# Performance work log

Hardware: AMD Instinct MI355X
Metric: run time of the kernel (lower is better)

Reference implementation:

```python
import jax, jax.numpy as jnp
import numpy as np

B = 4; D = H = W = 28; C = 192; NH = 6; WS = 7; SS = 3
L = D * H * W; N = WS ** 3; HD = C // NH


def _rel_index():
    c = np.stack(np.meshgrid(np.arange(WS), np.arange(WS), np.arange(WS), indexing='ij')).reshape(3, -1)
    r = c[:, :, None] - c[:, None, :] + (WS - 1)
    return jnp.asarray(r[0] * (2 * WS - 1) ** 2 + r[1] * (2 * WS - 1) + r[2])  # (N,N)


def _attn_mask():
    img = np.zeros((D, H, W), np.float32)
    sl = (slice(0, -WS), slice(-WS, -SS), slice(-SS, None))
    cnt = 0
    for d in sl:
        for h in sl:
            for w in sl:
                img[d, h, w] = cnt; cnt += 1
    mw = img.reshape(D // WS, WS, H // WS, WS, W // WS, WS).transpose(0, 2, 4, 1, 3, 5).reshape(-1, N)
    am = mw[:, None, :] - mw[:, :, None]
    return jnp.asarray(np.where(am != 0, -100.0, 0.0).astype(np.float32))  # (nW,N,N)

REL_IDX = _rel_index()
ATTN_MASK = _attn_mask()


def _ln(x, g, b):
    m = x.mean(-1, keepdims=True)
    v = ((x - m) ** 2).mean(-1, keepdims=True)
    return (x - m) / jnp.sqrt(v + 1e-5) * g + b


def _window_partition(x):  # (B,D,H,W,C) -> (B*nW, N, C)
    x = x.reshape(B, D // WS, WS, H // WS, WS, W // WS, WS, C)
    return x.transpose(0, 1, 3, 5, 2, 4, 6, 7).reshape(-1, N, C)


def _window_reverse(w):  # (B*nW, N, C) -> (B,D,H,W,C)
    x = w.reshape(B, D // WS, H // WS, W // WS, WS, WS, WS, C)
    return x.transpose(0, 1, 4, 2, 5, 3, 6, 7).reshape(B, D, H, W, C)


def setup_inputs() -> dict:
    key = jax.random.key(0)
    ks = jax.random.split(key, 8)
    s = 0.02
    return {
        'x': jax.random.normal(ks[0], (B, L, C), jnp.float32),
        'norm1_g': jnp.ones((C,), jnp.float32), 'norm1_b': jnp.zeros((C,), jnp.float32),
        'qkv_w': jax.random.normal(ks[1], (3 * C, C), jnp.float32) * s,
        'qkv_b': jnp.zeros((3 * C,), jnp.float32),
        'proj_w': jax.random.normal(ks[2], (C, C), jnp.float32) * s,
        'proj_b': jnp.zeros((C,), jnp.float32),
        'rel_table': jax.random.normal(ks[3], ((2 * WS - 1) ** 3, NH), jnp.float32) * s,
        'norm2_g': jnp.ones((C,), jnp.float32), 'norm2_b': jnp.zeros((C,), jnp.float32),
        'fc1_w': jax.random.normal(ks[4], (4 * C, C), jnp.float32) * s,
        'fc1_b': jnp.zeros((4 * C,), jnp.float32),
        'fc2_w': jax.random.normal(ks[5], (C, 4 * C), jnp.float32) * s,
        'fc2_b': jnp.zeros((C,), jnp.float32),
    }


def reference(x, norm1_g, norm1_b, qkv_w, qkv_b, proj_w, proj_b, rel_table,
              norm2_g, norm2_b, fc1_w, fc1_b, fc2_w, fc2_b):
    shortcut = x
    h = _ln(x, norm1_g, norm1_b).reshape(B, D, H, W, C)
    h = jnp.roll(h, (-SS, -SS, -SS), axis=(1, 2, 3))
    xw = _window_partition(h)                                  # (B_, N, C)
    B_ = xw.shape[0]
    qkv = (xw @ qkv_w.T + qkv_b).reshape(B_, N, 3, NH, HD).transpose(2, 0, 3, 1, 4)
    q, k, v = qkv[0], qkv[1], qkv[2]                           # (B_, NH, N, HD)
    attn = jnp.einsum('bhnd,bhmd->bhnm', q * (HD ** -0.5), k)
    bias = rel_table[REL_IDX].transpose(2, 0, 1)               # (NH, N, N)
    attn = attn + bias[None]
    nW = ATTN_MASK.shape[0]
    attn = (attn.reshape(B, nW, NH, N, N) + ATTN_MASK[None, :, None]).reshape(B_, NH, N, N)
    attn = jax.nn.softmax(attn, axis=-1)
    out = jnp.einsum('bhnm,bhmd->bhnd', attn, v).transpose(0, 2, 1, 3).reshape(B_, N, C)
    out = out @ proj_w.T + proj_b
    h = _window_reverse(out)
    h = jnp.roll(h, (SS, SS, SS), axis=(1, 2, 3)).reshape(B, L, C)
    x = shortcut + h
    y = _ln(x, norm2_g, norm2_b)
    y = jax.nn.gelu(y @ fc1_w.T + fc1_b, approximate=False)
    return x + (y @ fc2_w.T + fc2_b)
```

## Files before the change

kernel.cpp:

```cpp
#include <hip/hip_runtime.h>

#define DEV __device__ __forceinline__

typedef __bf16 bf16x8 __attribute__((ext_vector_type(8)));
typedef float f32x4 __attribute__((ext_vector_type(4)));

DEV float bflo(unsigned int u) { union { unsigned int x; float f; } c; c.x = u << 16; return c.f; }
DEV unsigned short f2bf(float f) {
  union { float f; unsigned int u; } c; c.f = f;
  unsigned int u = c.u;
  return (unsigned short)((u + 0x7fffu + ((u >> 16) & 1u)) >> 16);
}
DEV unsigned int pkbf(float a, float b) {
  unsigned int r;
  asm("v_cvt_pk_bf16_f32 %0, %1, %2" : "=v"(r) : "v"(a), "v"(b));
  return r;
}
DEV float gelu_fast(float y) {
  float y2 = y * y;
  float z = y * fmaf(y2, 0.10294348f, 2.30220842f);
  float e = __builtin_amdgcn_exp2f(z);
  float r = __builtin_amdgcn_rcpf(e + 1.0f);
  return fmaf(-y, r, y);
}

DEV void gload16(const void* g, void* l) {
  __builtin_amdgcn_global_load_lds((const __attribute__((address_space(1))) void*)g,
                                   (__attribute__((address_space(3))) void*)l, 16, 0, 0);
}

__global__ __launch_bounds__(256) void wconv_all(const float* __restrict__ s0,
                                                 const float* __restrict__ s1,
                                                 const float* __restrict__ s2,
                                                 const float* __restrict__ s3,
                                                 unsigned short* __restrict__ dst) {
  int i = blockIdx.x * 256 + threadIdx.x;
  const float* src; int off, real;
  if (i < 122880)      { src = s0; off = i;          real = 110592; }
  else if (i < 172032) { src = s1; off = i - 122880; real = 36864; }
  else if (i < 319488) { src = s2; off = i - 172032; real = 147456; }
  else                 { src = s3; off = i - 319488; real = 147456; }
  dst[i] = (off < real) ? f2bf(src[off]) : (unsigned short)0;
}

__global__ __launch_bounds__(256) void bmt_kernel(const float* __restrict__ rel_table,
                                                  unsigned short* __restrict__ bmt4) {
  int wth = blockIdx.x;
  int wt = wth / 6, h = wth - wt * 6;
  int r = blockIdx.y;
  unsigned short* row = bmt4 + (((size_t)wth * 88 + r) * 352) * 4;
  for (int q = threadIdx.x; q < 352; q += 256) {
    int mb_q = 0, cls_q = 0;
    bool qv = q < 343;
    if (qv) {
      int ii_q = q / 49, rem_q = q - ii_q * 49;
      int jj_q = rem_q / 7, ww_q = rem_q - jj_q * 7;
      mb_q = ii_q * 169 + jj_q * 13 + ww_q;
      int cd_q = (wt & 4) ? (ii_q < 4 ? 1 : 2) : 0;
      int ch_q = (wt & 2) ? (jj_q < 4 ? 1 : 2) : 0;
      int cw_q = (wt & 1) ? (ww_q < 4 ? 1 : 2) : 0;
      cls_q = cd_q * 9 + ch_q * 3 + cw_q;
    }
    unsigned short ov[4];
#pragma unroll
    for (int i = 0; i < 4; i++) {
      int kk = 4 * r + i;
      float v;
      if (kk >= 343) v = -30000.f;
      else if (!qv) v = 0.f;
      else {
        int ii_k = kk / 49, rem_k = kk - ii_k * 49;
        int jj_k = rem_k / 7, ww_k = rem_k - jj_k * 7;
        int mb_k = ii_k * 169 + jj_k * 13 + ww_k;
        int cd_k = (wt & 4) ? (ii_k < 4 ? 1 : 2) : 0;
        int ch_k = (wt & 2) ? (jj_k < 4 ? 1 : 2) : 0;
        int cw_k = (wt & 1) ? (ww_k < 4 ? 1 : 2) : 0;
        int cls_k = cd_k * 9 + ch_k * 3 + cw_k;
        v = rel_table[(mb_q - mb_k + 1098) * 6 + h] * 1.4426950408889634f;
        if (cls_q != cls_k) v -= 144.26950408889634f;
      }
      ov[i] = f2bf(v);
    }
    unsigned int lo = (unsigned)ov[0] | ((unsigned)ov[1] << 16);
    unsigned int hi = (unsigned)ov[2] | ((unsigned)ov[3] << 16);
    *(uint2*)(row + q * 4) = make_uint2(lo, hi);
  }
}

__global__ __launch_bounds__(256) void ln_kernel(const float* __restrict__ x,
                                                 const float* __restrict__ g,
                                                 const float* __restrict__ b,
                                                 unsigned short* __restrict__ out) {
  int row = (blockIdx.x << 2) + (threadIdx.x >> 6);
  int lane = threadIdx.x & 63;
  int w_ = row / 343, n_ = row - w_ * 343;
  int bb = w_ >> 6, wrem = w_ & 63;
  int wd = wrem >> 4, wh = (wrem >> 2) & 3, ww = wrem & 3;
  int ii = n_ / 49, rem = n_ - ii * 49;
  int jj = rem / 7, kk = rem - jj * 7;
  int d = wd * 7 + ii + 3; if (d >= 28) d -= 28;
  int hh = wh * 7 + jj + 3; if (hh >= 28) hh -= 28;
  int wb = ww * 7 + kk + 3; if (wb >= 28) wb -= 28;
  const float* xr = x + ((size_t)bb * 21952 + (d * 28 + hh) * 28 + wb) * 192;
  float v0 = xr[lane], v1 = xr[lane + 64], v2 = xr[lane + 128];
  float s = v0 + v1 + v2;
  float sq = v0 * v0 + v1 * v1 + v2 * v2;
#pragma unroll
  for (int o = 32; o > 0; o >>= 1) {
    s += __shfl_xor(s, o, 64);
    sq += __shfl_xor(sq, o, 64);
  }
  float mean = s * (1.0f / 192.0f);
  float var = sq * (1.0f / 192.0f) - mean * mean;
  float rstd = rsqrtf(var + 1e-5f);
  unsigned short* orow = out + (size_t)row * 192;
  orow[lane]       = f2bf((v0 - mean) * rstd * g[lane] + b[lane]);
  orow[lane + 64]  = f2bf((v1 - mean) * rstd * g[lane + 64] + b[lane + 64]);
  orow[lane + 128] = f2bf((v2 - mean) * rstd * g[lane + 128] + b[lane + 128]);
}

__global__ __launch_bounds__(256) void gemm_qkv(
    const unsigned short* __restrict__ A, const unsigned short* __restrict__ W,
    const float* __restrict__ bias,
    unsigned short* __restrict__ oq, unsigned short* __restrict__ okk,
    unsigned short* __restrict__ ov) {
  __shared__ __align__(16) unsigned short As[2][128 * 64];
  __shared__ __align__(16) unsigned short Bs[2][128 * 64];
  const int K = 192;
  const int orig = blockIdx.x;
  const int xcd = orig & 7, off = orig >> 3;
  const int wgid = (xcd < 6 ? xcd * 429 : 2574 + (xcd - 6) * 428) + off;
  const int by = wgid / 5, bx = wgid - by * 5;
  const int bm = by << 7, bn = bx << 7;

  const int tid = threadIdx.x;
  const int lane = tid & 63;
  const int wv = tid >> 6;
  const int wr = wv >> 1, wc = wv & 1;
  const int l15 = lane & 15, l4 = lane >> 4;
  const int srow = lane >> 3;
  const int scole = ((lane & 7) ^ srow) << 3;

  f32x4 acc[4][4];
#pragma unroll
  for (int a = 0; a < 4; a++)
#pragma unroll
    for (int b2 = 0; b2 < 4; b2++) acc[a][b2] = (f32x4){0.f, 0.f, 0.f, 0.f};

  auto stage = [&](int kt, int buf) {
#pragma unroll
    for (int i = 0; i < 4; i++) {
      int c = (i << 2) + wv;
      int row = (c << 3) + srow;
      gload16(A + (size_t)(bm + row) * K + (kt << 6) + scole, &As[buf][c << 9]);
      gload16(W + (size_t)(bn + row) * K + (kt << 6) + scole, &Bs[buf][c << 9]);
    }
  };

  stage(0, 0);
  int cur = 0;
  for (int kt = 0; kt < 3; ++kt) {
    if (kt < 2) {
      stage(kt + 1, cur ^ 1);
      asm volatile("s_waitcnt vmcnt(8)" ::: "memory");
    } else {
      asm volatile("s_waitcnt vmcnt(0)" ::: "memory");
    }
    __builtin_amdgcn_s_barrier();
    __builtin_amdgcn_sched_barrier(0);
#pragma unroll
    for (int ks = 0; ks < 2; ks++) {
      bf16x8 af[4], bfr[4];
#pragma unroll
      for (int fm = 0; fm < 4; fm++) {
        int r = (wr << 6) + (fm << 4) + l15;
        int c = (ks << 2) + l4;
        af[fm] = *(const bf16x8*)(&As[cur][(r << 6) + ((c ^ (r & 7)) << 3)]);
      }
#pragma unroll
      for (int fn = 0; fn < 4; fn++) {
        int r = (wc << 6) + (fn << 4) + l15;
        int c = (ks << 2) + l4;
        bfr[fn] = *(const bf16x8*)(&Bs[cur][(r << 6) + ((c ^ (r & 7)) << 3)]);
      }
#pragma unroll
      for (int fm = 0; fm < 4; fm++)
#pragma unroll
        for (int fn = 0; fn < 4; fn++)
          acc[fm][fn] = __builtin_amdgcn_mfma_f32_16x16x32_bf16(bfr[fn], af[fm], acc[fm][fn], 0, 0, 0);
    }
    if (kt < 2) {
      __builtin_amdgcn_sched_barrier(0);
      __builtin_amdgcn_s_barrier();
      cur ^= 1;
    }
  }

#pragma unroll
  for (int fm = 0; fm < 4; fm++) {
    int gr = bm + (wr << 6) + (fm << 4) + l15;
    int w_ = gr / 343, n_ = gr - w_ * 343;
#pragma unroll
    for (int fn = 0; fn < 4; fn++) {
      int gc0 = bn + (wc << 6) + (fn << 4) + (l4 << 2);
      if (gc0 < 576) {
        float4 bv = *(const float4*)(bias + gc0);
        float v0 = acc[fm][fn][0] + bv.x, v1 = acc[fm][fn][1] + bv.y;
        float v2 = acc[fm][fn][2] + bv.z, v3 = acc[fm][fn][3] + bv.w;
        int which = gc0 / 192;
        int cc3 = gc0 - which * 192;
        int hh2 = cc3 >> 5, dd0 = cc3 & 31;
        size_t offo = ((size_t)(w_ * 6 + hh2) * 343 + n_) * 32 + dd0;
        if (which == 0) {
          const float sc = 0.17677669529663687f * 1.4426950408889634f;
          *(uint2*)(oq + offo) = make_uint2(pkbf(v0 * sc, v1 * sc), pkbf(v2 * sc, v3 * sc));
        } else if (which == 1) {
          *(uint2*)(okk + offo) = make_uint2(pkbf(v0, v1), pkbf(v2, v3));
        } else {
          *(uint2*)(ov + offo) = make_uint2(pkbf(v0, v1), pkbf(v2, v3));
        }
      }
    }
  }
}

__global__ __launch_bounds__(256) void gemm_proj_ln(
    const unsigned short* __restrict__ A, const unsigned short* __restrict__ W,
    const float* __restrict__ bias, const float* __restrict__ x,
    const float* __restrict__ g2, const float* __restrict__ b2,
    unsigned short* __restrict__ xnew, unsigned short* __restrict__ xw2) {
  __shared__ __align__(16) char smem[65536];
  unsigned short (*As)[64 * 64] = (unsigned short (*)[64 * 64])smem;
  unsigned short (*Bs)[192 * 64] = (unsigned short (*)[192 * 64])(smem + 16384);
  float* red = (float*)smem;

  const int tid = threadIdx.x;
  const int lane = tid & 63;
  const int wv = tid >> 6;
  const int bm = blockIdx.x << 6;
  const int l15 = lane & 15, l4 = lane >> 4;
  const int srow = lane >> 3;
  const int scole = ((lane & 7) ^ srow) << 3;
  const int K = 192;

  f32x4 acc[4][3];
#pragma unroll
  for (int a = 0; a < 4; a++)
#pragma unroll
    for (int b_ = 0; b_ < 3; b_++) acc[a][b_] = (f32x4){0.f, 0.f, 0.f, 0.f};

  auto stage = [&](int kt, int buf) {
#pragma unroll
    for (int i = 0; i < 2; i++) {
      int c = (i << 2) + wv;
      gload16(A + (size_t)(bm + (c << 3) + srow) * K + (kt << 6) + scole, &As[buf][c << 9]);
    }
#pragma unroll
    for (int i = 0; i < 6; i++) {
      int c = (i << 2) + wv;
      gload16(W + (size_t)((c << 3) + srow) * K + (kt << 6) + scole, &Bs[buf][c << 9]);
    }
  };

  stage(0, 0);
  int cur = 0;
  for (int kt = 0; kt < 3; ++kt) {
    if (kt < 2) {
      stage(kt + 1, cur ^ 1);
      asm volatile("s_waitcnt vmcnt(8)" ::: "memory");
    } else {
      asm volatile("s_waitcnt vmcnt(0)" ::: "memory");
    }
    __builtin_amdgcn_s_barrier();
    __builtin_amdgcn_sched_barrier(0);
#pragma unroll
    for (int ks = 0; ks < 2; ks++) {
      bf16x8 af[4], bfr[3];
#pragma unroll
      for (int fm = 0; fm < 4; fm++) {
        int r = (fm << 4) + l15;
        int c = (ks << 2) + l4;
        af[fm] = *(const bf16x8*)(&As[cur][(r << 6) + ((c ^ (r & 7)) << 3)]);
      }
#pragma unroll
      for (int fn = 0; fn < 3; fn++) {
        int r = (wv * 48) + (fn << 4) + l15;
        int c = (ks << 2) + l4;
        bfr[fn] = *(const bf16x8*)(&Bs[cur][(r << 6) + ((c ^ (r & 7)) << 3)]);
      }
#pragma unroll
      for (int fm = 0; fm < 4; fm++)
#pragma unroll
        for (int fn = 0; fn < 3; fn++)
          acc[fm][fn] = __builtin_amdgcn_mfma_f32_16x16x32_bf16(bfr[fn], af[fm], acc[fm][fn], 0, 0, 0);
    }
    if (kt < 2) {
      __builtin_amdgcn_sched_barrier(0);
      __builtin_amdgcn_s_barrier();
      cur ^= 1;
    }
  }

  size_t orow[4];
#pragma unroll
  for (int fm = 0; fm < 4; fm++) {
    int gr = bm + (fm << 4) + l15;
    int w_ = gr / 343, n_ = gr - w_ * 343;
    int bb = w_ >> 6, wrem = w_ & 63;
    int wd = wrem >> 4, wh = (wrem >> 2) & 3, ww = wrem & 3;
    int ii = n_ / 49, rem = n_ - ii * 49;
    int jj = rem / 7, kk = rem - jj * 7;
    int d = wd * 7 + ii + 3; if (d >= 28) d -= 28;
    int hh = wh * 7 + jj + 3; if (hh >= 28) hh -= 28;
    int wb = ww * 7 + kk + 3; if (wb >= 28) wb -= 28;
    orow[fm] = ((size_t)bb * 21952 + (d * 28 + hh) * 28 + wb) * 192;
  }
  float ps[4], psq[4];
#pragma unroll
  for (int fm = 0; fm < 4; fm++) {
    float s = 0.f, sq = 0.f;
#pragma unroll
    for (int fn = 0; fn < 3; fn++) {
      int gc0 = wv * 48 + (fn << 4) + (l4 << 2);
      float4 bv = *(const float4*)(bias + gc0);
      float4 xv = *(const float4*)(x + orow[fm] + gc0);
      acc[fm][fn][0] += bv.x + xv.x;
      acc[fm][fn][1] += bv.y + xv.y;
      acc[fm][fn][2] += bv.z + xv.z;
      acc[fm][fn][3] += bv.w + xv.w;
#pragma unroll
      for (int i = 0; i < 4; i++) {
        float v = acc[fm][fn][i];
        s += v; sq += v * v;
      }
    }
    ps[fm] = s; psq[fm] = sq;
  }
#pragma unroll
  for (int fm = 0; fm < 4; fm++) {
    ps[fm] += __shfl_xor(ps[fm], 16, 64);
    ps[fm] += __shfl_xor(ps[fm], 32, 64);
    psq[fm] += __shfl_xor(psq[fm], 16, 64);
    psq[fm] += __shfl_xor(psq[fm], 32, 64);
  }
  __syncthreads();
  if (l4 == 0) {
#pragma unroll
    for (int fm = 0; fm < 4; fm++) {
      int tr = (fm << 4) + l15;
      red[tr * 8 + wv] = ps[fm];
      red[tr * 8 + 4 + wv] = psq[fm];
    }
  }
  __syncthreads();
  if (tid < 64) {
    float s = red[tid * 8] + red[tid * 8 + 1] + red[tid * 8 + 2] + red[tid * 8 + 3];
    float sq = red[tid * 8 + 4] + red[tid * 8 + 5] + red[tid * 8 + 6] + red[tid * 8 + 7];
    float mean = s * (1.0f / 192.0f);
    float var = sq * (1.0f / 192.0f) - mean * mean;
    red[tid * 8] = mean;
    red[tid * 8 + 1] = rsqrtf(var + 1e-5f);
  }
  __syncthreads();
#pragma unroll
  for (int fm = 0; fm < 4; fm++) {
    int tr = (fm << 4) + l15;
    float mean = red[tr * 8], rstd = red[tr * 8 + 1];
#pragma unroll
    for (int fn = 0; fn < 3; fn++) {
      int gc0 = wv * 48 + (fn << 4) + (l4 << 2);
      float4 gv = *(const float4*)(g2 + gc0);
      float4 b2v = *(const float4*)(b2 + gc0);
      float v0 = acc[fm][fn][0], v1 = acc[fm][fn][1];
      float v2 = acc[fm][fn][2], v3 = acc[fm][fn][3];
      *(uint2*)(xnew + orow[fm] + gc0) = make_uint2(pkbf(v0, v1), pkbf(v2, v3));
      float y0 = (v0 - mean) * rstd * gv.x + b2v.x;
      float y1 = (v1 - mean) * rstd * gv.y + b2v.y;
      float y2 = (v2 - mean) * rstd * gv.z + b2v.z;
      float y3 = (v3 - mean) * rstd * gv.w + b2v.w;
      *(uint2*)(xw2 + orow[fm] + gc0) = make_uint2(pkbf(y0, y1), pkbf(y2, y3));
    }
  }
}

__global__ __launch_bounds__(256) void mlp_fused(
    const unsigned short* __restrict__ A,
    const unsigned short* __restrict__ W1,
    const float* __restrict__ b1,
    const unsigned short* __restrict__ W2,
    const float* __restrict__ b2,
    const unsigned short* __restrict__ residb,
    float* __restrict__ out) {
  __shared__ __align__(16) unsigned short As[64 * 192];
  __shared__ __align__(16) unsigned short Hs[64 * 264];
  const int tid = threadIdx.x, lane = tid & 63, wv = tid >> 6;
  const int l15 = lane & 15, l4 = lane >> 4;
  const int bm = blockIdx.x << 6;

#pragma unroll
  for (int i = 0; i < 6; i++) {
    int idx = i * 256 + tid;
    int r = idx / 24, c = idx - r * 24;
    gload16(A + (size_t)(bm + r) * 192 + ((c ^ (r & 7)) << 3), As + r * 192 + (c << 3));
  }

  f32x4 acc2[4][3];
#pragma unroll
  for (int a = 0; a < 4; a++)
#pragma unroll
    for (int b_ = 0; b_ < 3; b_++) acc2[a][b_] = (f32x4){0.f, 0.f, 0.f, 0.f};

  asm volatile("s_waitcnt vmcnt(0)" ::: "memory");
  __syncthreads();

  for (int cc = 0; cc < 3; cc++) {
    f32x4 acc1[4][4];
#pragma unroll
    for (int a = 0; a < 4; a++)
#pragma unroll
      for (int b_ = 0; b_ < 4; b_++) acc1[a][b_] = (f32x4){0.f, 0.f, 0.f, 0.f};
#pragma unroll
    for (int ks = 0; ks < 6; ks++) {
      bf16x8 af[4], bf[4];
#pragma unroll
      for (int fm = 0; fm < 4; fm++) {
        int r = (fm << 4) + l15;
        int ch = (ks << 2) + l4;
        af[fm] = *(const bf16x8*)(As + r * 192 + ((ch ^ (r & 7)) << 3));
      }
#pragma unroll
      for (int fn = 0; fn < 4; fn++) {
        int hrow = (cc << 8) + (wv << 6) + (fn << 4) + l15;
        bf[fn] = *(const bf16x8*)(W1 + (size_t)hrow * 192 + (ks << 5) + (l4 << 3));
      }
#pragma unroll
      for (int fm = 0; fm < 4; fm++)
#pragma unroll
        for (int fn = 0; fn < 4; fn++)
          acc1[fm][fn] = __builtin_amdgcn_mfma_f32_16x16x32_bf16(bf[fn], af[fm], acc1[fm][fn], 0, 0, 0);
    }
    __syncthreads();
#pragma unroll
    for (int fm = 0; fm < 4; fm++) {
      int r = (fm << 4) + l15;
#pragma unroll
      for (int fn = 0; fn < 4; fn++) {
        int hc = (wv << 6) + (fn << 4) + (l4 << 2);
        float4 bv = *(const float4*)(b1 + (cc << 8) + hc);
        float g0 = gelu_fast(acc1[fm][fn][0] + bv.x);
        float g1 = gelu_fast(acc1[fm][fn][1] + bv.y);
        float g2 = gelu_fast(acc1[fm][fn][2] + bv.z);
        float g3 = gelu_fast(acc1[fm][fn][3] + bv.w);
        *(uint2*)(Hs + r * 264 + hc) = make_uint2(pkbf(g0, g1), pkbf(g2, g3));
      }
    }
    __syncthreads();
#pragma unroll
    for (int ks = 0; ks < 8; ks++) {
      bf16x8 hf[4], wf[3];
#pragma unroll
      for (int fm = 0; fm < 4; fm++) {
        int r = (fm << 4) + l15;
        hf[fm] = *(const bf16x8*)(Hs + r * 264 + (ks << 5) + (l4 << 3));
      }
#pragma unroll
      for (int fn = 0; fn < 3; fn++) {
        int j = wv * 48 + (fn << 4) + l15;
        wf[fn] = *(const bf16x8*)(W2 + (size_t)j * 768 + (cc << 8) + (ks << 5) + (l4 << 3));
      }
#pragma unroll
      for (int fm = 0; fm < 4; fm++)
#pragma unroll
        for (int fn = 0; fn < 3; fn++)
          acc2[fm][fn] = __builtin_amdgcn_mfma_f32_16x16x32_bf16(wf[fn], hf[fm], acc2[fm][fn], 0, 0, 0);
    }
  }

#pragma unroll
  for (int fm = 0; fm < 4; fm++) {
    int gr = bm + (fm << 4) + l15;
#pragma unroll
    for (int fn = 0; fn < 3; fn++) {
      int gc0 = wv * 48 + (fn << 4) + (l4 << 2);
      size_t oi = (size_t)gr * 192 + gc0;
      float4 bv = *(const float4*)(b2 + gc0);
      uint2 rb = *(const uint2*)(residb + oi);
      float4 o;
      o.x = acc2[fm][fn][0] + bv.x + bflo(rb.x & 0xffffu);
      o.y = acc2[fm][fn][1] + bv.y + bflo(rb.x >> 16);
      o.z = acc2[fm][fn][2] + bv.z + bflo(rb.y & 0xffffu);
      o.w = acc2[fm][fn][3] + bv.w + bflo(rb.y >> 16);
      *(float4*)(out + oi) = o;
    }
  }
}

__global__ __launch_bounds__(256) void attn_mfma(const unsigned short* __restrict__ q,
                                                 const unsigned short* __restrict__ k,
                                                 const unsigned short* __restrict__ v,
                                                 const unsigned short* __restrict__ bmt4,
                                                 unsigned short* __restrict__ out) {
  __shared__ __align__(16) unsigned short Ks[352 * 32];
  __shared__ __align__(16) unsigned short Vt[32 * 360];

  const int blk = blockIdx.x;
  const int h_ = blk >> 8;
  const int idx = blk & 255;
  const int cums[8] = {0, 108, 144, 180, 192, 228, 240, 252};
  int c = (idx >= 108) + (idx >= 144) + (idx >= 180) + (idx >= 192) +
          (idx >= 228) + (idx >= 240) + (idx >= 252);
  int r0 = idx - cums[c];
  int sh = (c & 2) ? 1 : 3, sw = (c & 1) ? 1 : 3;
  int p = ((c & 4) ? 1 : 3) * sh * sw;
  int b = r0 / p, q2 = r0 - b * p;
  int wd, wh, ww;
  if (c & 4) wd = 3; else { wd = q2 / (sh * sw); q2 -= wd * sh * sw; }
  if (c & 2) wh = 3; else { wh = q2 / sw; q2 -= wh * sw; }
  ww = (c & 1) ? 3 : q2;
  const int w_ = b * 64 + wd * 16 + wh * 4 + ww;
  const int wt = c;
  const int blkqkv = w_ * 6 + h_;

  const int t = threadIdx.x, lane = t & 63, wv = t >> 6;
  const int l15 = lane & 15, l4 = lane >> 4;
  const unsigned short* Qb = q + (size_t)blkqkv * (343 * 32);
  const unsigned short* Kb = k + (size_t)blkqkv * (343 * 32);
  const unsigned short* Vb = v + (size_t)blkqkv * (343 * 32);
  const unsigned short* bm4 = bmt4 + ((size_t)(wt * 6 + h_) * 88) * 352 * 4;

  for (int cc = t; cc < 1408; cc += 256) {
    int r = cc >> 2, ch = cc & 3;
    int swc = ch ^ ((r >> 1) & 3);
    uint4 val = make_uint4(0, 0, 0, 0);
    if (r < 343) val = *(const uint4*)(Kb + r * 32 + ch * 8);
    *(uint4*)(Ks + r * 32 + swc * 8) = val;
  }
#pragma unroll
  for (int ch = 0; ch < 4; ch++) {
    for (int n = t; n < 343; n += 256) {
      union { uint4 u4; unsigned short us[8]; } val;
      val.u4 = *(const uint4*)(Vb + n * 32 + ch * 8);
#pragma unroll
      for (int j = 0; j < 8; j++) Vt[(ch * 8 + j) * 360 + n] = val.us[j];
    }
  }
  for (int cc = t; cc < 288; cc += 256) {
    int d = cc / 9, n = 343 + (cc - d * 9);
    Vt[d * 360 + n] = 0;
  }
  __syncthreads();

  const int ksw = (l4 ^ ((l15 >> 1) & 3)) << 3;

  for (int tq = wv; tq < 22; tq += 4) {
    int qrow = tq * 16 + l15; if (qrow > 342) qrow = 342;
    bf16x8 qf = *(const bf16x8*)(Qb + qrow * 32 + l4 * 8);

    unsigned int u0[22], u1[22];
    float lsum = 0.f;
#pragma unroll
    for (int kt = 0; kt < 22; kt++) {
      bf16x8 kf = *(const bf16x8*)(Ks + (kt * 16 + l15) * 32 + ksw);
      f32x4 s = __builtin_amdgcn_mfma_f32_16x16x32_bf16(kf, qf, (f32x4){0.f, 0.f, 0.f, 0.f}, 0, 0, 0);
      const unsigned short* bp = bm4 + ((size_t)((kt << 2) + l4) * 352 + (tq << 4) + l15) * 4;
      uint2 bv = *(const uint2*)bp;
      float p0 = __builtin_amdgcn_exp2f(s[0] + bflo(bv.x & 0xffffu));
      float p1 = __builtin_amdgcn_exp2f(s[1] + bflo(bv.x >> 16));
      float p2 = __builtin_amdgcn_exp2f(s[2] + bflo(bv.y & 0xffffu));
      float p3 = __builtin_amdgcn_exp2f(s[3] + bflo(bv.y >> 16));
      lsum += (p0 + p1) + (p2 + p3);
      asm("v_cvt_pk_bf16_f32 %0, %1, %2" : "=v"(u0[kt]) : "v"(p0), "v"(p1));
      asm("v_cvt_pk_bf16_f32 %0, %1, %2" : "=v"(u1[kt]) : "v"(p2), "v"(p3));
    }
    lsum += __shfl_xor(lsum, 16, 64);
    lsum += __shfl_xor(lsum, 32, 64);
    float inv = 1.0f / lsum;

    f32x4 oacc0 = (f32x4){0.f, 0.f, 0.f, 0.f};
    f32x4 oacc1 = (f32x4){0.f, 0.f, 0.f, 0.f};
#pragma unroll
    for (int ck = 0; ck < 11; ck++) {
      unsigned int dw[4];
#pragma unroll
      for (int d = 0; d < 4; d++) {
        int src = l15 + 16 * ((d >> 1) + 2 * (l4 & 1));
        unsigned int x = __shfl((d & 1) ? u1[2 * ck] : u0[2 * ck], src, 64);
        unsigned int y = __shfl((d & 1) ? u1[2 * ck + 1] : u0[2 * ck + 1], src, 64);
        dw[d] = (l4 < 2) ? x : y;
      }
      union { unsigned int u[4]; bf16x8 v; } pc;
      pc.u[0] = dw[0]; pc.u[1] = dw[1]; pc.u[2] = dw[2]; pc.u[3] = dw[3];
      bf16x8 vf0 = *(const bf16x8*)(Vt + (size_t)l15 * 360 + ck * 32 + l4 * 8);
      bf16x8 vf1 = *(const bf16x8*)(Vt + (size_t)(16 + l15) * 360 + ck * 32 + l4 * 8);
      oacc0 = __builtin_amdgcn_mfma_f32_16x16x32_bf16(vf0, pc.v, oacc0, 0, 0, 0);
      oacc1 = __builtin_amdgcn_mfma_f32_16x16x32_bf16(vf1, pc.v, oacc1, 0, 0, 0);
    }

    int qg = tq * 16 + l15;
    if (qg < 343) {
      unsigned short* orow = out + ((size_t)w_ * 343 + qg) * 192 + h_ * 32;
      *(uint2*)(orow + (l4 << 2)) =
          make_uint2(pkbf(oacc0[0] * inv, oacc0[1] * inv), pkbf(oacc0[2] * inv, oacc0[3] * inv));
      *(uint2*)(orow + 16 + (l4 << 2)) =
          make_uint2(pkbf(oacc1[0] * inv, oacc1[1] * inv), pkbf(oacc1[2] * inv, oacc1[3] * inv));
    }
  }
}

extern "C" void kernel_launch(void* const* d_in, const int* in_sizes, int n_in,
                              void* d_out, int out_size, void* d_ws, size_t ws_size,
                              hipStream_t stream) {
  const float* x      = (const float*)d_in[0];
  const float* n1g    = (const float*)d_in[1];
  const float* n1b    = (const float*)d_in[2];
  const float* qkv_w  = (const float*)d_in[3];
  const float* qkv_b  = (const float*)d_in[4];
  const float* proj_w = (const float*)d_in[5];
  const float* proj_b = (const float*)d_in[6];
  const float* rel_t  = (const float*)d_in[7];
  const float* n2g    = (const float*)d_in[8];
  const float* n2b    = (const float*)d_in[9];
  const float* fc1_w  = (const float*)d_in[10];
  const float* fc1_b  = (const float*)d_in[11];
  const float* fc2_w  = (const float*)d_in[12];
  const float* fc2_b  = (const float*)d_in[13];

  char* ws = (char*)d_ws;
  if (ws_size < 237060096ull) return;
  unsigned short* WQKV  = (unsigned short*)(ws);
  unsigned short* WPROJ = (unsigned short*)(ws + 245760);
  unsigned short* WFC1  = (unsigned short*)(ws + 344064);
  unsigned short* WFC2  = (unsigned short*)(ws + 638976);
  unsigned short* XW    = (unsigned short*)(ws + 1032192);
  unsigned short* Q_    = (unsigned short*)(ws + 34750464);
  unsigned short* K_    = (unsigned short*)(ws + 68468736);
  unsigned short* V_    = (unsigned short*)(ws + 102187008);
  unsigned short* BMT4  = (unsigned short*)(ws + 135925248);
  unsigned short* XNEWb = (unsigned short*)(ws + 34750464);
  unsigned short* XW2   = (unsigned short*)(ws + 68468736);
  float* OUT = (float*)d_out;

  wconv_all<<<2016, 256, 0, stream>>>(qkv_w, proj_w, fc1_w, fc2_w, WQKV);

  bmt_kernel<<<dim3(48, 88), 256, 0, stream>>>(rel_t, BMT4);

  ln_kernel<<<21952, 256, 0, stream>>>(x, n1g, n1b, XW);

  gemm_qkv<<<3430, 256, 0, stream>>>(XW, WQKV, qkv_b, Q_, K_, V_);

  attn_mfma<<<1536, 256, 0, stream>>>(Q_, K_, V_, BMT4, XW);

  gemm_proj_ln<<<1372, 256, 0, stream>>>(XW, WPROJ, proj_b, x, n2g, n2b, XNEWb, XW2);

  mlp_fused<<<1372, 256, 0, stream>>>(XW2, WFC1, fc1_b, WFC2, fc2_b, XNEWb, OUT);
}
```

Measured before the change: 352.2 us.

## Fuse projection+LN2 GEMM with MLP kernel, keeping tile on-chip

Merges the proj+residual+LayerNorm kernel with the fused MLP kernel, so the normalized tile stays in shared memory and the residual stays in registers. This removes the global write and re-read of the two bf16 intermediates and one kernel launch. The output is written directly to the un-shifted token positions. To fit shared memory, the projection GEMM drops its double-buffered staging and the MLP hidden chunk shrinks from 256 to 128 columns, which lowers overlap and doubles the chunk-loop iterations.

```diff
diff --git a/kernel.cpp b/kernel.cpp
--- a/kernel.cpp
+++ b/kernel.cpp
@@ -224,24 +224,24 @@
   }
 }
 
-__global__ __launch_bounds__(256) void gemm_proj_ln(
-    const unsigned short* __restrict__ A, const unsigned short* __restrict__ W,
-    const float* __restrict__ bias, const float* __restrict__ x,
+__global__ __launch_bounds__(256) void proj_mlp(
+    const unsigned short* __restrict__ A,
+    const unsigned short* __restrict__ Wp, const float* __restrict__ bp,
+    const float* __restrict__ x,
     const float* __restrict__ g2, const float* __restrict__ b2,
-    unsigned short* __restrict__ xnew, unsigned short* __restrict__ xw2) {
-  __shared__ __align__(16) char smem[65536];
-  unsigned short (*As)[64 * 64] = (unsigned short (*)[64 * 64])smem;
-  unsigned short (*Bs)[192 * 64] = (unsigned short (*)[192 * 64])(smem + 16384);
-  float* red = (float*)smem;
-
-  const int tid = threadIdx.x;
-  const int lane = tid & 63;
-  const int wv = tid >> 6;
+    const unsigned short* __restrict__ W1, const float* __restrict__ b1,
+    const unsigned short* __restrict__ W2, const float* __restrict__ b2b,
+    float* __restrict__ out) {
+  __shared__ __align__(16) char smem[43008];
+  unsigned short* pBs  = (unsigned short*)smem;
+  unsigned short* pAs  = (unsigned short*)(smem + 24576);
+  unsigned short* xw2s = (unsigned short*)smem;
+  unsigned short* Hs   = (unsigned short*)(smem + 24576);
+  float* red = (float*)(smem + 24576);
+
+  const int tid = threadIdx.x, lane = tid & 63, wv = tid >> 6;
+  const int l15 = lane & 15, l4 = lane >> 4;
   const int bm = blockIdx.x << 6;
-  const int l15 = lane & 15, l4 = lane >> 4;
-  const int srow = lane >> 3;
-  const int scole = ((lane & 7) ^ srow) << 3;
-  const int K = 192;
 
   f32x4 acc[4][3];
 #pragma unroll
@@ -249,30 +249,22 @@
 #pragma unroll
     for (int b_ = 0; b_ < 3; b_++) acc[a][b_] = (f32x4){0.f, 0.f, 0.f, 0.f};
 
-  auto stage = [&](int kt, int buf) {
+  for (int kt = 0; kt < 3; ++kt) {
+    __syncthreads();
 #pragma unroll
     for (int i = 0; i < 2; i++) {
-      int c = (i << 2) + wv;
-      gload16(A + (size_t)(bm + (c << 3) + srow) * K + (kt << 6) + scole, &As[buf][c << 9]);
+      int u = (i << 8) + tid;
+      int r = u >> 3, ch = u & 7;
+      gload16(A + (size_t)(bm + r) * 192 + (kt << 6) + ((ch ^ (r & 7)) << 3), pAs + (u << 3));
     }
 #pragma unroll
     for (int i = 0; i < 6; i++) {
-      int c = (i << 2) + wv;
-      gload16(W + (size_t)((c << 3) + srow) * K + (kt << 6) + scole, &Bs[buf][c << 9]);
-    }
-  };
-
-  stage(0, 0);
-  int cur = 0;
-  for (int kt = 0; kt < 3; ++kt) {
-    if (kt < 2) {
-      stage(kt + 1, cur ^ 1);
-      asm volatile("s_waitcnt vmcnt(8)" ::: "memory");
-    } else {
-      asm volatile("s_waitcnt vmcnt(0)" ::: "memory");
-    }
-    __builtin_amdgcn_s_barrier();
-    __builtin_amdgcn_sched_barrier(0);
+      int u = (i << 8) + tid;
+      int r = u >> 3, ch = u & 7;
+      gload16(Wp + (size_t)r * 192 + (kt << 6) + ((ch ^ (r & 7)) << 3), pBs + (u << 3));
+    }
+    asm volatile("s_waitcnt vmcnt(0)" ::: "memory");
+    __syncthreads();
 #pragma unroll
     for (int ks = 0; ks < 2; ks++) {
       bf16x8 af[4], bfr[3];
@@ -280,13 +272,13 @@
       for (int fm = 0; fm < 4; fm++) {
         int r = (fm << 4) + l15;
         int c = (ks << 2) + l4;
-        af[fm] = *(const bf16x8*)(&As[cur][(r << 6) + ((c ^ (r & 7)) << 3)]);
+        af[fm] = *(const bf16x8*)(pAs + (r << 6) + ((c ^ (r & 7)) << 3));
       }
 #pragma unroll
       for (int fn = 0; fn < 3; fn++) {
-        int r = (wv * 48) + (fn << 4) + l15;
+        int rr = wv * 48 + (fn << 4) + l15;
         int c = (ks << 2) + l4;
-        bfr[fn] = *(const bf16x8*)(&Bs[cur][(r << 6) + ((c ^ (r & 7)) << 3)]);
+        bfr[fn] = *(const bf16x8*)(pBs + (rr << 6) + ((c ^ (rr & 7)) << 3));
       }
 #pragma unroll
       for (int fm = 0; fm < 4; fm++)
@@ -294,14 +286,9 @@
         for (int fn = 0; fn < 3; fn++)
           acc[fm][fn] = __builtin_amdgcn_mfma_f32_16x16x32_bf16(bfr[fn], af[fm], acc[fm][fn], 0, 0, 0);
     }
-    if (kt < 2) {
-      __builtin_amdgcn_sched_barrier(0);
-      __builtin_amdgcn_s_barrier();
-      cur ^= 1;
-    }
-  }
-
-  size_t orow[4];
+  }
+
+  int orow[4];
 #pragma unroll
   for (int fm = 0; fm < 4; fm++) {
     int gr = bm + (fm << 4) + l15;
@@ -313,7 +300,7 @@
     int d = wd * 7 + ii + 3; if (d >= 28) d -= 28;
     int hh = wh * 7 + jj + 3; if (hh >= 28) hh -= 28;
     int wb = ww * 7 + kk + 3; if (wb >= 28) wb -= 28;
-    orow[fm] = ((size_t)bb * 21952 + (d * 28 + hh) * 28 + wb) * 192;
+    orow[fm] = ((bb * 21952 + (d * 28 + hh) * 28 + wb) * 192);
   }
   float ps[4], psq[4];
 #pragma unroll
@@ -322,8 +309,8 @@
 #pragma unroll
     for (int fn = 0; fn < 3; fn++) {
       int gc0 = wv * 48 + (fn << 4) + (l4 << 2);
-      float4 bv = *(const float4*)(bias + gc0);
-      float4 xv = *(const float4*)(x + orow[fm] + gc0);
+      float4 bv = *(const float4*)(bp + gc0);
+      float4 xv = *(const float4*)(x + (size_t)orow[fm] + gc0);
       acc[fm][fn][0] += bv.x + xv.x;
       acc[fm][fn][1] += bv.y + xv.y;
       acc[fm][fn][2] += bv.z + xv.z;
@@ -362,6 +349,7 @@
     red[tid * 8 + 1] = rsqrtf(var + 1e-5f);
   }
   __syncthreads();
+  unsigned int xnb[4][3][2];
 #pragma unroll
   for (int fm = 0; fm < 4; fm++) {
     int tr = (fm << 4) + l15;
@@ -373,36 +361,18 @@
       float4 b2v = *(const float4*)(b2 + gc0);
       float v0 = acc[fm][fn][0], v1 = acc[fm][fn][1];
       float v2 = acc[fm][fn][2], v3 = acc[fm][fn][3];
-      *(uint2*)(xnew + orow[fm] + gc0) = make_uint2(pkbf(v0, v1), pkbf(v2, v3));
+      xnb[fm][fn][0] = pkbf(v0, v1);
+      xnb[fm][fn][1] = pkbf(v2, v3);
       float y0 = (v0 - mean) * rstd * gv.x + b2v.x;
       float y1 = (v1 - mean) * rstd * gv.y + b2v.y;
       float y2 = (v2 - mean) * rstd * gv.z + b2v.z;
       float y3 = (v3 - mean) * rstd * gv.w + b2v.w;
-      *(uint2*)(xw2 + orow[fm] + gc0) = make_uint2(pkbf(y0, y1), pkbf(y2, y3));
-    }
-  }
-}
-
-__global__ __launch_bounds__(256) void mlp_fused(
-    const unsigned short* __restrict__ A,
-    const unsigned short* __restrict__ W1,
-    const float* __restrict__ b1,
-    const unsigned short* __restrict__ W2,
-    const float* __restrict__ b2,
-    const unsigned short* __restrict__ residb,
-    float* __restrict__ out) {
-  __shared__ __align__(16) unsigned short As[64 * 192];
-  __shared__ __align__(16) unsigned short Hs[64 * 264];
-  const int tid = threadIdx.x, lane = tid & 63, wv = tid >> 6;
-  const int l15 = lane & 15, l4 = lane >> 4;
-  const int bm = blockIdx.x << 6;
-
-#pragma unroll
-  for (int i = 0; i < 6; i++) {
-    int idx = i * 256 + tid;
-    int r = idx / 24, c = idx - r * 24;
-    gload16(A + (size_t)(bm + r) * 192 + ((c ^ (r & 7)) << 3), As + r * 192 + (c << 3));
-  }
+      int ch = gc0 >> 3;
+      *(uint2*)(xw2s + tr * 192 + ((ch ^ (tr & 7)) << 3) + (gc0 & 7)) =
+          make_uint2(pkbf(y0, y1), pkbf(y2, y3));
+    }
+  }
+  __syncthreads();
 
   f32x4 acc2[4][3];
 #pragma unroll
@@ -410,87 +380,82 @@
 #pragma unroll
     for (int b_ = 0; b_ < 3; b_++) acc2[a][b_] = (f32x4){0.f, 0.f, 0.f, 0.f};
 
-  asm volatile("s_waitcnt vmcnt(0)" ::: "memory");
-  __syncthreads();
-
-  for (int cc = 0; cc < 3; cc++) {
-    f32x4 acc1[4][4];
-#pragma unroll
-    for (int a = 0; a < 4; a++)
-#pragma unroll
-      for (int b_ = 0; b_ < 4; b_++) acc1[a][b_] = (f32x4){0.f, 0.f, 0.f, 0.f};
+  for (int cc = 0; cc < 6; cc++) {
+    f32x4 acc1[4][2];
+#pragma unroll
+    for (int a = 0; a < 4; a++) {
+      acc1[a][0] = (f32x4){0.f, 0.f, 0.f, 0.f};
+      acc1[a][1] = (f32x4){0.f, 0.f, 0.f, 0.f};
+    }
 #pragma unroll
     for (int ks = 0; ks < 6; ks++) {
-      bf16x8 af[4], bf[4];
+      bf16x8 af[4], w1f[2];
 #pragma unroll
       for (int fm = 0; fm < 4; fm++) {
         int r = (fm << 4) + l15;
         int ch = (ks << 2) + l4;
-        af[fm] = *(const bf16x8*)(As + r * 192 + ((ch ^ (r & 7)) << 3));
-      }
-#pragma unroll
-      for (int fn = 0; fn < 4; fn++) {
-        int hrow = (cc << 8) + (wv << 6) + (fn << 4) + l15;
-        bf[fn] = *(const bf16x8*)(W1 + (size_t)hrow * 192 + (ks << 5) + (l4 << 3));
+        af[fm] = *(const bf16x8*)(xw2s + r * 192 + ((ch ^ (r & 7)) << 3));
+      }
+#pragma unroll
+      for (int fn = 0; fn < 2; fn++) {
+        int hrow = (cc << 7) + (wv << 5) + (fn << 4) + l15;
+        w1f[fn] = *(const bf16x8*)(W1 + (size_t)hrow * 192 + (ks << 5) + (l4 << 3));
       }
 #pragma unroll
       for (int fm = 0; fm < 4; fm++)
 #pragma unroll
-        for (int fn = 0; fn < 4; fn++)
-          acc1[fm][fn] = __builtin_amdgcn_mfma_f32_16x16x32_bf16(bf[fn], af[fm], acc1[fm][fn], 0, 0, 0);
+        for (int fn = 0; fn < 2; fn++)
+          acc1[fm][fn] = __builtin_amdgcn_mfma_f32_16x16x32_bf16(w1f[fn], af[fm], acc1[fm][fn], 0, 0, 0);
     }
     __syncthreads();
 #pragma unroll
     for (int fm = 0; fm < 4; fm++) {
       int r = (fm << 4) + l15;
 #pragma unroll
-      for (int fn = 0; fn < 4; fn++) {
-        int hc = (wv << 6) + (fn << 4) + (l4 << 2);
-        float4 bv = *(const float4*)(b1 + (cc << 8) + hc);
+      for (int fn = 0; fn < 2; fn++) {
+        int hc = (wv << 5) + (fn << 4) + (l4 << 2);
+        float4 bv = *(const float4*)(b1 + (cc << 7) + hc);
         float g0 = gelu_fast(acc1[fm][fn][0] + bv.x);
         float g1 = gelu_fast(acc1[fm][fn][1] + bv.y);
-        float g2 = gelu_fast(acc1[fm][fn][2] + bv.z);
+        float g2_ = gelu_fast(acc1[fm][fn][2] + bv.z);
         float g3 = gelu_fast(acc1[fm][fn][3] + bv.w);
-        *(uint2*)(Hs + r * 264 + hc) = make_uint2(pkbf(g0, g1), pkbf(g2, g3));
+        *(uint2*)(Hs + r * 136 + hc) = make_uint2(pkbf(g0, g1), pkbf(g2_, g3));
       }
     }
     __syncthreads();
 #pragma unroll
-    for (int ks = 0; ks < 8; ks++) {
-      bf16x8 hf[4], wf[3];
+    for (int ks = 0; ks < 4; ks++) {
+      bf16x8 hf[4], w2f[3];
 #pragma unroll
       for (int fm = 0; fm < 4; fm++) {
         int r = (fm << 4) + l15;
-        hf[fm] = *(const bf16x8*)(Hs + r * 264 + (ks << 5) + (l4 << 3));
+        hf[fm] = *(const bf16x8*)(Hs + r * 136 + (ks << 5) + (l4 << 3));
       }
 #pragma unroll
       for (int fn = 0; fn < 3; fn++) {
         int j = wv * 48 + (fn << 4) + l15;
-        wf[fn] = *(const bf16x8*)(W2 + (size_t)j * 768 + (cc << 8) + (ks << 5) + (l4 << 3));
+        w2f[fn] = *(const bf16x8*)(W2 + (size_t)j * 768 + (cc << 7) + (ks << 5) + (l4 << 3));
       }
 #pragma unroll
       for (int fm = 0; fm < 4; fm++)
 #pragma unroll
         for (int fn = 0; fn < 3; fn++)
-          acc2[fm][fn] = __builtin_amdgcn_mfma_f32_16x16x32_bf16(wf[fn], hf[fm], acc2[fm][fn], 0, 0, 0);
+          acc2[fm][fn] = __builtin_amdgcn_mfma_f32_16x16x32_bf16(w2f[fn], hf[fm], acc2[fm][fn], 0, 0, 0);
     }
   }
 
 #pragma unroll
   for (int fm = 0; fm < 4; fm++) {
-    int gr = bm + (fm << 4) + l15;
 #pragma unroll
     for (int fn = 0; fn < 3; fn++) {
       int gc0 = wv * 48 + (fn << 4) + (l4 << 2);
-      size_t oi = (size_t)gr * 192 + gc0;
-      float4 bv = *(const float4*)(b2 + gc0);
-      uint2 rb = *(const uint2*)(residb + oi);
+      float4 bv = *(const float4*)(b2b + gc0);
       float4 o;
-      o.x = acc2[fm][fn][0] + bv.x + bflo(rb.x & 0xffffu);
-      o.y = acc2[fm][fn][1] + bv.y + bflo(rb.x >> 16);
-      o.z = acc2[fm][fn][2] + bv.z + bflo(rb.y & 0xffffu);
-      o.w = acc2[fm][fn][3] + bv.w + bflo(rb.y >> 16);
-      *(float4*)(out + oi) = o;
+      o.x = acc2[fm][fn][0] + bv.x + bflo(xnb[fm][fn][0] & 0xffffu);
+      o.y = acc2[fm][fn][1] + bv.y + bflo(xnb[fm][fn][0] >> 16);
+      o.z = acc2[fm][fn][2] + bv.z + bflo(xnb[fm][fn][1] & 0xffffu);
+      o.w = acc2[fm][fn][3] + bv.w + bflo(xnb[fm][fn][1] >> 16);
+      *(float4*)(out + (size_t)orow[fm] + gc0) = o;
     }
   }
 }
@@ -626,7 +591,7 @@
   const float* fc2_b  = (const float*)d_in[13];
 
   char* ws = (char*)d_ws;
-  if (ws_size < 237060096ull) return;
+  if (ws_size < 147820032ull) return;
   unsigned short* WQKV  = (unsigned short*)(ws);
   unsigned short* WPROJ = (unsigned short*)(ws + 245760);
   unsigned short* WFC1  = (unsigned short*)(ws + 344064);
@@ -636,8 +601,6 @@
   unsigned short* K_    = (unsigned short*)(ws + 68468736);
   unsigned short* V_    = (unsigned short*)(ws + 102187008);
   unsigned short* BMT4  = (unsigned short*)(ws + 135925248);
-  unsigned short* XNEWb = (unsigned short*)(ws + 34750464);
-  unsigned short* XW2   = (unsigned short*)(ws + 68468736);
   float* OUT = (float*)d_out;
 
   wconv_all<<<2016, 256, 0, stream>>>(qkv_w, proj_w, fc1_w, fc2_w, WQKV);
@@ -650,7 +613,6 @@
 
   attn_mfma<<<1536, 256, 0, stream>>>(Q_, K_, V_, BMT4, XW);
 
-  gemm_proj_ln<<<1372, 256, 0, stream>>>(XW, WPROJ, proj_b, x, n2g, n2b, XNEWb, XW2);
-
-  mlp_fused<<<1372, 256, 0, stream>>>(XW2, WFC1, fc1_b, WFC2, fc2_b, XNEWb, OUT);
-}
+  proj_mlp<<<1372, 256, 0, stream>>>(XW, WPROJ, proj_b, x, n2g, n2b,
+                                     WFC1, fc1_b, WFC2, fc2_b, OUT);
+}
```

Result: faster. 326.1 us (-7.4%).
